# Performance work log

Measured on AMD Instinct MI355X. Metric: run time of the kernel, lower is better.

Reference implementation:

```python
import jax, jax.numpy as jnp
import numpy as np

NUM_HEADS = 64  # init kwarg


def _split_heads(x, num_heads):
    # torch: x.view(N, num_heads, head_size).permute(0, 2, 1) -> [N, head_size, num_heads]
    n, hidden = x.shape
    head_size = hidden // num_heads
    return x.reshape(n, num_heads, head_size).transpose(0, 2, 1)


def setup_inputs() -> dict:
    key = jax.random.key(0)
    kq, kk, kv = jax.random.split(key, 3)
    N, H = 4096, 4096
    q = jax.random.normal(kq, (N, H), dtype=jnp.float32)
    k = jax.random.normal(kk, (N, H), dtype=jnp.float32)
    v = jax.random.normal(kv, (N, H), dtype=jnp.float32)
    return {"q": q, "k": k, "v": v}


def reference(q, k, v):
    n, hidden = q.shape
    qh = _split_heads(q, NUM_HEADS)  # [N, d, h] with d=head_size, h=num_heads
    kh = _split_heads(k, NUM_HEADS)
    vh = _split_heads(v, NUM_HEADS)
    # scores: contraction over the num_heads axis (faithful to the original code)
    scores = jnp.einsum('ndh,neh->nde', qh, kh)      # [N, d, d]
    probs = jax.nn.softmax(scores, axis=-1)           # softmax over last dim, no scaling
    out = jnp.einsum('nde,neh->ndh', probs, vh)       # [N, d, h]
    # permute(0,2,1) then flatten -> [N, hidden]
    return out.transpose(0, 2, 1).reshape(n, hidden)
```

## Files before the change

### kernel.cpp

```cpp
#include <hip/hip_runtime.h>
#include <hip/hip_bf16.h>

typedef __bf16 bf16x8 __attribute__((ext_vector_type(8)));
typedef float  f32x4  __attribute__((ext_vector_type(4)));
typedef short  s16x8  __attribute__((ext_vector_type(8)));
typedef unsigned short u16;

static __device__ __forceinline__ u16 f2bf_rne(float f) {
  union { float f; unsigned u; } x; x.f = f;
  unsigned r = x.u + 0x7fffu + ((x.u >> 16) & 1u);
  return (u16)(r >> 16);
}

static __device__ __forceinline__ void splitbf(float f, short& hi, short& lo) {
  union { float f; unsigned u; } x; x.f = f;
  hi = (short)(x.u >> 16);
  union { unsigned u; float f; } h; h.u = x.u & 0xffff0000u;
  union { float f; unsigned u; } y; y.f = f - h.f;
  lo = (short)(y.u >> 16);
}

#define GLD_LDS16(g, l)                                                        \
  __builtin_amdgcn_global_load_lds(                                            \
      (const __attribute__((address_space(1))) void*)(g),                      \
      (__attribute__((address_space(3))) void*)(l), 16, 0, 0)

__global__ __launch_bounds__(256, 3)
void attn64_kernel(const float* __restrict__ q, const float* __restrict__ k,
                   const float* __restrict__ v, float* __restrict__ out)
{
  __shared__ float ldsQ[4096];
  __shared__ float ldsK[4096];
  __shared__ float ldsV[4096];

  const int tid  = threadIdx.x;
  const int wid  = tid >> 6;
  const int lane = tid & 63;
  const int quad = lane >> 4;
  const int lo   = lane & 15;
  const int row  = blockIdx.x;

  const float* qrow = q + (size_t)row * 4096;
  const float* krow = k + (size_t)row * 4096;
  const float* vrow = v + (size_t)row * 4096;
  float*       orow = out + (size_t)row * 4096;

  {
    const int hl = lane >> 4;
    const int e4 = (lane & 15) << 2;
#pragma unroll
    for (int i = 0; i < 4; ++i) {
      const int c = wid * 4 + i;
      const int h = c * 4 + hl;
      const int seQK = e4 ^ (((h >> 3) & 1) << 4);
      const int seV  = e4 ^ ((h & 15) << 2);
      GLD_LDS16(qrow + h * 64 + seQK, &ldsQ[c * 256]);
      GLD_LDS16(krow + h * 64 + seQK, &ldsK[c * 256]);
      GLD_LDS16(vrow + h * 64 + seV,  &ldsV[c * 256]);
    }
  }
  __syncthreads();

  s16x8 qh[2], ql[2];
  {
    const int dcol = wid * 16 + lo;
#pragma unroll
    for (int ks = 0; ks < 2; ++ks)
#pragma unroll
      for (int j = 0; j < 8; ++j) {
        const int h = ks * 32 + quad * 8 + j;
        float x = ldsQ[h * 64 + (dcol ^ ((quad & 1) << 4))];
        short hh, ll; splitbf(x, hh, ll);
        qh[ks][j] = hh; ql[ks][j] = ll;
      }
  }

  f32x4 acc[4];
#pragma unroll
  for (int et = 0; et < 4; ++et) acc[et] = (f32x4){0.f, 0.f, 0.f, 0.f};

#pragma unroll
  for (int et = 0; et < 4; ++et)
#pragma unroll
    for (int ks = 0; ks < 2; ++ks) {
      s16x8 kh, kl;
#pragma unroll
      for (int j = 0; j < 8; ++j) {
        const int h = ks * 32 + quad * 8 + j;
        float x = ldsK[h * 64 + ((lo + 16 * et) ^ ((quad & 1) << 4))];
        short hh, ll; splitbf(x, hh, ll);
        kh[j] = hh; kl[j] = ll;
      }
      bf16x8 ah = __builtin_bit_cast(bf16x8, qh[ks]);
      bf16x8 al = __builtin_bit_cast(bf16x8, ql[ks]);
      bf16x8 bh = __builtin_bit_cast(bf16x8, kh);
      bf16x8 bl = __builtin_bit_cast(bf16x8, kl);
      acc[et] = __builtin_amdgcn_mfma_f32_16x16x32_bf16(ah, bh, acc[et], 0, 0, 0);
      acc[et] = __builtin_amdgcn_mfma_f32_16x16x32_bf16(ah, bl, acc[et], 0, 0, 0);
      acc[et] = __builtin_amdgcn_mfma_f32_16x16x32_bf16(al, bh, acc[et], 0, 0, 0);
    }

#pragma unroll
  for (int r = 0; r < 4; ++r) {
    float m = fmaxf(fmaxf(acc[0][r], acc[1][r]), fmaxf(acc[2][r], acc[3][r]));
#pragma unroll
    for (int off = 1; off < 16; off <<= 1) m = fmaxf(m, __shfl_xor(m, off));
    float s = 0.f;
#pragma unroll
    for (int et = 0; et < 4; ++et) {
      float e0 = __expf(acc[et][r] - m);
      acc[et][r] = e0;
      s += e0;
    }
#pragma unroll
    for (int off = 1; off < 16; off <<= 1) s += __shfl_xor(s, off);
    float rs = 1.0f / s;
#pragma unroll
    for (int et = 0; et < 4; ++et) acc[et][r] *= rs;
  }

  __syncthreads();

  float* P = ldsK;
#pragma unroll
  for (int r = 0; r < 4; ++r) {
    const int d   = wid * 16 + quad * 4 + r;
    const int swz = (d & 15) << 2;
#pragma unroll
    for (int et = 0; et < 4; ++et)
      P[d * 64 + ((lo + 16 * et) ^ swz)] = acc[et][r];
  }

  f32x4 acc2[4];
#pragma unroll
  for (int mt = 0; mt < 4; ++mt) acc2[mt] = (f32x4){0.f, 0.f, 0.f, 0.f};

#pragma unroll
  for (int ks = 0; ks < 2; ++ks) {
    const int eb = quad * 8 + ks * 32;

    const int dmine = wid * 16 + lo;
    const int pswz  = lo << 2;
    f32x4 p0 = *(const f32x4*)&P[dmine * 64 + (eb ^ pswz)];
    f32x4 p1 = *(const f32x4*)&P[dmine * 64 + ((eb + 4) ^ pswz)];
    s16x8 tp;
#pragma unroll
    for (int j = 0; j < 4; ++j) {
      tp[j]     = (short)f2bf_rne(p0[j]);
      tp[4 + j] = (short)f2bf_rne(p1[j]);
    }
    bf16x8 bp = __builtin_bit_cast(bf16x8, tp);

#pragma unroll
    for (int mt = 0; mt < 4; ++mt) {
      const int h    = lo + 16 * mt;
      const int vswz = lo << 2;
      f32x4 v0 = *(const f32x4*)&ldsV[h * 64 + (eb ^ vswz)];
      f32x4 v1 = *(const f32x4*)&ldsV[h * 64 + ((eb + 4) ^ vswz)];
      s16x8 tv;
#pragma unroll
      for (int j = 0; j < 4; ++j) {
        tv[j]     = (short)f2bf_rne(v0[j]);
        tv[4 + j] = (short)f2bf_rne(v1[j]);
      }
      bf16x8 av = __builtin_bit_cast(bf16x8, tv);
      acc2[mt] = __builtin_amdgcn_mfma_f32_16x16x32_bf16(av, bp, acc2[mt], 0, 0, 0);
    }
  }

#pragma unroll
  for (int mt = 0; mt < 4; ++mt)
#pragma unroll
    for (int r = 0; r < 4; ++r) {
      const int h = 16 * mt + quad * 4 + r;
      orow[h * 64 + wid * 16 + lo] = acc2[mt][r];
    }
}

extern "C" void kernel_launch(void* const* d_in, const int* in_sizes, int n_in,
                              void* d_out, int out_size, void* d_ws, size_t ws_size,
                              hipStream_t stream) {
  const float* q = (const float*)d_in[0];
  const float* k = (const float*)d_in[1];
  const float* v = (const float*)d_in[2];
  float* o = (float*)d_out;
  hipLaunchKernelGGL(attn64_kernel, dim3(4096), dim3(256), 0, stream, q, k, v, o);
}
```

Measured before the change: 213.4 us.

## Process eight rows per block with double-buffered async Q/K staging and register V

Each 512-thread block now handles 8 rows, two at a time over 4 iterations. While one LDS buffer is being computed on, Q/K for the next pair of rows stream into the other buffer through global_load_lds, and V is loaded straight into registers instead of going through LDS. The aim is to hide global-load latency behind MFMA and softmax work and to cut per-block launch overhead. The cost is more LDS (128KB per block, so fewer resident blocks), high register pressure from holding V in registers, and hand-written barriers and waitcnt that are easy to get wrong.

```diff
diff --git a/kernel.cpp b/kernel.cpp
--- a/kernel.cpp
+++ b/kernel.cpp
@@ -25,156 +25,183 @@
       (const __attribute__((address_space(1))) void*)(g),                      \
       (__attribute__((address_space(3))) void*)(l), 16, 0, 0)
 
-__global__ __launch_bounds__(256, 3)
+__global__ __launch_bounds__(512, 2)
 void attn64_kernel(const float* __restrict__ q, const float* __restrict__ k,
                    const float* __restrict__ v, float* __restrict__ out)
 {
-  __shared__ float ldsQ[4096];
-  __shared__ float ldsK[4096];
-  __shared__ float ldsV[4096];
+  __shared__ float lds[2][2][2][4096];
 
   const int tid  = threadIdx.x;
   const int wid  = tid >> 6;
   const int lane = tid & 63;
   const int quad = lane >> 4;
   const int lo   = lane & 15;
-  const int row  = blockIdx.x;
-
-  const float* qrow = q + (size_t)row * 4096;
-  const float* krow = k + (size_t)row * 4096;
-  const float* vrow = v + (size_t)row * 4096;
-  float*       orow = out + (size_t)row * 4096;
-
-  {
+  const int rw   = wid >> 2;
+  const int wq   = wid & 3;
+  const int rowBase = blockIdx.x * 8;
+
+  auto stage = [&](int t, int b) {
     const int hl = lane >> 4;
     const int e4 = (lane & 15) << 2;
 #pragma unroll
-    for (int i = 0; i < 4; ++i) {
-      const int c = wid * 4 + i;
-      const int h = c * 4 + hl;
-      const int seQK = e4 ^ (((h >> 3) & 1) << 4);
-      const int seV  = e4 ^ ((h & 15) << 2);
-      GLD_LDS16(qrow + h * 64 + seQK, &ldsQ[c * 256]);
-      GLD_LDS16(krow + h * 64 + seQK, &ldsK[c * 256]);
-      GLD_LDS16(vrow + h * 64 + seV,  &ldsV[c * 256]);
-    }
+    for (int i = 0; i < 8; ++i) {
+      const int c   = wid * 8 + i;
+      const int sec = c >> 4;
+      const int c4  = c & 15;
+      const int h   = c4 * 4 + hl;
+      const int se  = e4 ^ (((h >> 3) & 1) << 4);
+      const float* src = ((sec & 1) ? k : q)
+                       + (size_t)(rowBase + t * 2 + (sec >> 1)) * 4096
+                       + h * 64 + se;
+      GLD_LDS16(src, &lds[b][sec & 1][sec >> 1][c4 * 256]);
+    }
+  };
+
+  f32x4 xv[8][2];
+  auto loadV = [&](int t) {
+    const float* vrow = v + (size_t)(rowBase + t * 2 + rw) * 4096;
+#pragma unroll
+    for (int ks = 0; ks < 2; ++ks)
+#pragma unroll
+      for (int mt = 0; mt < 4; ++mt) {
+        const float* p = vrow + (lo + 16 * mt) * 64 + quad * 8 + ks * 32;
+        xv[ks * 4 + mt][0] = *(const f32x4*)p;
+        xv[ks * 4 + mt][1] = *(const f32x4*)(p + 4);
+      }
+  };
+
+  stage(0, 0);
+  loadV(0);
+
+  for (int t = 0; t < 4; ++t) {
+    const int b = t & 1;
+
+    asm volatile("s_waitcnt vmcnt(0)\n\ts_barrier" ::: "memory");
+    __builtin_amdgcn_sched_barrier(0);
+
+    bf16x8 av[8];
+#pragma unroll
+    for (int i = 0; i < 8; ++i) {
+      s16x8 tv;
+#pragma unroll
+      for (int j = 0; j < 4; ++j) {
+        tv[j]     = (short)f2bf_rne(xv[i][0][j]);
+        tv[4 + j] = (short)f2bf_rne(xv[i][1][j]);
+      }
+      av[i] = __builtin_bit_cast(bf16x8, tv);
+    }
+
+    if (t < 3) {
+      stage(t + 1, b ^ 1);
+      loadV(t + 1);
+    }
+
+    const float* ldsQ = &lds[b][0][rw][0];
+    float*       ldsK = &lds[b][1][rw][0];
+
+    s16x8 qh[2], ql[2];
+    {
+      const int dcol = wq * 16 + lo;
+#pragma unroll
+      for (int ks = 0; ks < 2; ++ks)
+#pragma unroll
+        for (int j = 0; j < 8; ++j) {
+          const int h = ks * 32 + quad * 8 + j;
+          float x = ldsQ[h * 64 + (dcol ^ ((quad & 1) << 4))];
+          short hh, ll; splitbf(x, hh, ll);
+          qh[ks][j] = hh; ql[ks][j] = ll;
+        }
+    }
+
+    f32x4 acc[4];
+#pragma unroll
+    for (int et = 0; et < 4; ++et) acc[et] = (f32x4){0.f, 0.f, 0.f, 0.f};
+
+#pragma unroll
+    for (int et = 0; et < 4; ++et)
+#pragma unroll
+      for (int ks = 0; ks < 2; ++ks) {
+        s16x8 kh, kl;
+#pragma unroll
+        for (int j = 0; j < 8; ++j) {
+          const int h = ks * 32 + quad * 8 + j;
+          float x = ldsK[h * 64 + ((lo + 16 * et) ^ ((quad & 1) << 4))];
+          short hh, ll; splitbf(x, hh, ll);
+          kh[j] = hh; kl[j] = ll;
+        }
+        bf16x8 ah = __builtin_bit_cast(bf16x8, qh[ks]);
+        bf16x8 al = __builtin_bit_cast(bf16x8, ql[ks]);
+        bf16x8 bh = __builtin_bit_cast(bf16x8, kh);
+        bf16x8 bl = __builtin_bit_cast(bf16x8, kl);
+        acc[et] = __builtin_amdgcn_mfma_f32_16x16x32_bf16(ah, bh, acc[et], 0, 0, 0);
+        acc[et] = __builtin_amdgcn_mfma_f32_16x16x32_bf16(ah, bl, acc[et], 0, 0, 0);
+        acc[et] = __builtin_amdgcn_mfma_f32_16x16x32_bf16(al, bh, acc[et], 0, 0, 0);
+      }
+
+#pragma unroll
+    for (int r = 0; r < 4; ++r) {
+      float m = fmaxf(fmaxf(acc[0][r], acc[1][r]), fmaxf(acc[2][r], acc[3][r]));
+#pragma unroll
+      for (int off = 1; off < 16; off <<= 1) m = fmaxf(m, __shfl_xor(m, off));
+      float s = 0.f;
+#pragma unroll
+      for (int et = 0; et < 4; ++et) {
+        float e0 = __expf(acc[et][r] - m);
+        acc[et][r] = e0;
+        s += e0;
+      }
+#pragma unroll
+      for (int off = 1; off < 16; off <<= 1) s += __shfl_xor(s, off);
+      float rs = 1.0f / s;
+#pragma unroll
+      for (int et = 0; et < 4; ++et) acc[et][r] *= rs;
+    }
+
+    asm volatile("s_barrier" ::: "memory");
+    __builtin_amdgcn_sched_barrier(0);
+
+    float* P = ldsK;
+#pragma unroll
+    for (int r = 0; r < 4; ++r) {
+      const int d   = wq * 16 + quad * 4 + r;
+      const int swz = (d & 15) << 2;
+#pragma unroll
+      for (int et = 0; et < 4; ++et)
+        P[d * 64 + ((lo + 16 * et) ^ swz)] = acc[et][r];
+    }
+
+    f32x4 acc2[4];
+#pragma unroll
+    for (int mt = 0; mt < 4; ++mt) acc2[mt] = (f32x4){0.f, 0.f, 0.f, 0.f};
+
+#pragma unroll
+    for (int ks = 0; ks < 2; ++ks) {
+      const int eb    = quad * 8 + ks * 32;
+      const int dmine = wq * 16 + lo;
+      const int pswz  = lo << 2;
+      f32x4 p0 = *(const f32x4*)&P[dmine * 64 + (eb ^ pswz)];
+      f32x4 p1 = *(const f32x4*)&P[dmine * 64 + ((eb + 4) ^ pswz)];
+      s16x8 tp;
+#pragma unroll
+      for (int j = 0; j < 4; ++j) {
+        tp[j]     = (short)f2bf_rne(p0[j]);
+        tp[4 + j] = (short)f2bf_rne(p1[j]);
+      }
+      bf16x8 bp = __builtin_bit_cast(bf16x8, tp);
+#pragma unroll
+      for (int mt = 0; mt < 4; ++mt)
+        acc2[mt] = __builtin_amdgcn_mfma_f32_16x16x32_bf16(av[ks * 4 + mt], bp, acc2[mt], 0, 0, 0);
+    }
+
+    float* orow = out + (size_t)(rowBase + t * 2 + rw) * 4096;
+#pragma unroll
+    for (int mt = 0; mt < 4; ++mt)
+#pragma unroll
+      for (int r = 0; r < 4; ++r) {
+        const int h = 16 * mt + quad * 4 + r;
+        orow[h * 64 + wq * 16 + lo] = acc2[mt][r];
+      }
   }
-  __syncthreads();
-
-  s16x8 qh[2], ql[2];
-  {
-    const int dcol = wid * 16 + lo;
-#pragma unroll
-    for (int ks = 0; ks < 2; ++ks)
-#pragma unroll
-      for (int j = 0; j < 8; ++j) {
-        const int h = ks * 32 + quad * 8 + j;
-        float x = ldsQ[h * 64 + (dcol ^ ((quad & 1) << 4))];
-        short hh, ll; splitbf(x, hh, ll);
-        qh[ks][j] = hh; ql[ks][j] = ll;
-      }
-  }
-
-  f32x4 acc[4];
-#pragma unroll
-  for (int et = 0; et < 4; ++et) acc[et] = (f32x4){0.f, 0.f, 0.f, 0.f};
-
-#pragma unroll
-  for (int et = 0; et < 4; ++et)
-#pragma unroll
-    for (int ks = 0; ks < 2; ++ks) {
-      s16x8 kh, kl;
-#pragma unroll
-      for (int j = 0; j < 8; ++j) {
-        const int h = ks * 32 + quad * 8 + j;
-        float x = ldsK[h * 64 + ((lo + 16 * et) ^ ((quad & 1) << 4))];
-        short hh, ll; splitbf(x, hh, ll);
-        kh[j] = hh; kl[j] = ll;
-      }
-      bf16x8 ah = __builtin_bit_cast(bf16x8, qh[ks]);
-      bf16x8 al = __builtin_bit_cast(bf16x8, ql[ks]);
-      bf16x8 bh = __builtin_bit_cast(bf16x8, kh);
-      bf16x8 bl = __builtin_bit_cast(bf16x8, kl);
-      acc[et] = __builtin_amdgcn_mfma_f32_16x16x32_bf16(ah, bh, acc[et], 0, 0, 0);
-      acc[et] = __builtin_amdgcn_mfma_f32_16x16x32_bf16(ah, bl, acc[et], 0, 0, 0);
-      acc[et] = __builtin_amdgcn_mfma_f32_16x16x32_bf16(al, bh, acc[et], 0, 0, 0);
-    }
-
-#pragma unroll
-  for (int r = 0; r < 4; ++r) {
-    float m = fmaxf(fmaxf(acc[0][r], acc[1][r]), fmaxf(acc[2][r], acc[3][r]));
-#pragma unroll
-    for (int off = 1; off < 16; off <<= 1) m = fmaxf(m, __shfl_xor(m, off));
-    float s = 0.f;
-#pragma unroll
-    for (int et = 0; et < 4; ++et) {
-      float e0 = __expf(acc[et][r] - m);
-      acc[et][r] = e0;
-      s += e0;
-    }
-#pragma unroll
-    for (int off = 1; off < 16; off <<= 1) s += __shfl_xor(s, off);
-    float rs = 1.0f / s;
-#pragma unroll
-    for (int et = 0; et < 4; ++et) acc[et][r] *= rs;
-  }
-
-  __syncthreads();
-
-  float* P = ldsK;
-#pragma unroll
-  for (int r = 0; r < 4; ++r) {
-    const int d   = wid * 16 + quad * 4 + r;
-    const int swz = (d & 15) << 2;
-#pragma unroll
-    for (int et = 0; et < 4; ++et)
-      P[d * 64 + ((lo + 16 * et) ^ swz)] = acc[et][r];
-  }
-
-  f32x4 acc2[4];
-#pragma unroll
-  for (int mt = 0; mt < 4; ++mt) acc2[mt] = (f32x4){0.f, 0.f, 0.f, 0.f};
-
-#pragma unroll
-  for (int ks = 0; ks < 2; ++ks) {
-    const int eb = quad * 8 + ks * 32;
-
-    const int dmine = wid * 16 + lo;
-    const int pswz  = lo << 2;
-    f32x4 p0 = *(const f32x4*)&P[dmine * 64 + (eb ^ pswz)];
-    f32x4 p1 = *(const f32x4*)&P[dmine * 64 + ((eb + 4) ^ pswz)];
-    s16x8 tp;
-#pragma unroll
-    for (int j = 0; j < 4; ++j) {
-      tp[j]     = (short)f2bf_rne(p0[j]);
-      tp[4 + j] = (short)f2bf_rne(p1[j]);
-    }
-    bf16x8 bp = __builtin_bit_cast(bf16x8, tp);
-
-#pragma unroll
-    for (int mt = 0; mt < 4; ++mt) {
-      const int h    = lo + 16 * mt;
-      const int vswz = lo << 2;
-      f32x4 v0 = *(const f32x4*)&ldsV[h * 64 + (eb ^ vswz)];
-      f32x4 v1 = *(const f32x4*)&ldsV[h * 64 + ((eb + 4) ^ vswz)];
-      s16x8 tv;
-#pragma unroll
-      for (int j = 0; j < 4; ++j) {
-        tv[j]     = (short)f2bf_rne(v0[j]);
-        tv[4 + j] = (short)f2bf_rne(v1[j]);
-      }
-      bf16x8 av = __builtin_bit_cast(bf16x8, tv);
-      acc2[mt] = __builtin_amdgcn_mfma_f32_16x16x32_bf16(av, bp, acc2[mt], 0, 0, 0);
-    }
-  }
-
-#pragma unroll
-  for (int mt = 0; mt < 4; ++mt)
-#pragma unroll
-    for (int r = 0; r < 4; ++r) {
-      const int h = 16 * mt + quad * 4 + r;
-      orow[h * 64 + wid * 16 + lo] = acc2[mt][r];
-    }
 }
 
 extern "C" void kernel_launch(void* const* d_in, const int* in_sizes, int n_in,
@@ -184,5 +211,5 @@
   const float* k = (const float*)d_in[1];
   const float* v = (const float*)d_in[2];
   float* o = (float*)d_out;
-  hipLaunchKernelGGL(attn64_kernel, dim3(4096), dim3(256), 0, stream, q, k, v, o);
-}
+  hipLaunchKernelGGL(attn64_kernel, dim3(512), dim3(512), 0, stream, q, k, v, o);
+}
```

Result: slower. 233.3 us (+9.3%).

## Load V directly into registers, drop V LDS buffer, raise occupancy

Applied to the files above, without the earlier changes.

V is no longer staged through shared memory. Each thread issues direct global vector loads of its V fragments into registers right after the Q/K LDS fill, and converts them to bf16 just before the second MFMA stage. This cuts LDS use per block from 48KB to 32KB, and launch bounds are raised to 4 blocks per CU so more rows can be in flight. The cost is 64 extra VGPRs held live across the QK^T and softmax phases, which may cause spills or limit occupancy under the tighter register budget. The direct V loads are also less coalesced than the previous LDS-staged path.

```diff
diff --git a/kernel.cpp b/kernel.cpp
--- a/kernel.cpp
+++ b/kernel.cpp
@@ -25,13 +25,12 @@
       (const __attribute__((address_space(1))) void*)(g),                      \
       (__attribute__((address_space(3))) void*)(l), 16, 0, 0)
 
-__global__ __launch_bounds__(256, 3)
+__global__ __launch_bounds__(256, 4)
 void attn64_kernel(const float* __restrict__ q, const float* __restrict__ k,
                    const float* __restrict__ v, float* __restrict__ out)
 {
   __shared__ float ldsQ[4096];
   __shared__ float ldsK[4096];
-  __shared__ float ldsV[4096];
 
   const int tid  = threadIdx.x;
   const int wid  = tid >> 6;
@@ -49,17 +48,28 @@
     const int hl = lane >> 4;
     const int e4 = (lane & 15) << 2;
 #pragma unroll
-    for (int i = 0; i < 4; ++i) {
-      const int c = wid * 4 + i;
-      const int h = c * 4 + hl;
-      const int seQK = e4 ^ (((h >> 3) & 1) << 4);
-      const int seV  = e4 ^ ((h & 15) << 2);
-      GLD_LDS16(qrow + h * 64 + seQK, &ldsQ[c * 256]);
-      GLD_LDS16(krow + h * 64 + seQK, &ldsK[c * 256]);
-      GLD_LDS16(vrow + h * 64 + seV,  &ldsV[c * 256]);
+    for (int i = 0; i < 8; ++i) {
+      const int c   = wid * 8 + i;
+      const int sec = c >> 4;
+      const int c4  = c & 15;
+      const int h   = c4 * 4 + hl;
+      const int se  = e4 ^ (((h >> 3) & 1) << 4);
+      const float* src = (sec ? krow : qrow) + h * 64 + se;
+      GLD_LDS16(src, (sec ? ldsK : ldsQ) + c4 * 256);
     }
   }
   __syncthreads();
+
+  f32x4 xv[8][2];
+#pragma unroll
+  for (int ks = 0; ks < 2; ++ks)
+#pragma unroll
+    for (int mt = 0; mt < 4; ++mt) {
+      const float* p = vrow + (lo + 16 * mt) * 64 + quad * 8 + ks * 32;
+      xv[ks * 4 + mt][0] = *(const f32x4*)p;
+      xv[ks * 4 + mt][1] = *(const f32x4*)(p + 4);
+    }
+  __builtin_amdgcn_sched_barrier(0);
 
   s16x8 qh[2], ql[2];
   {
@@ -121,6 +131,18 @@
 
   __syncthreads();
 
+  bf16x8 av[8];
+#pragma unroll
+  for (int i = 0; i < 8; ++i) {
+    s16x8 tv;
+#pragma unroll
+    for (int j = 0; j < 4; ++j) {
+      tv[j]     = (short)f2bf_rne(xv[i][0][j]);
+      tv[4 + j] = (short)f2bf_rne(xv[i][1][j]);
+    }
+    av[i] = __builtin_bit_cast(bf16x8, tv);
+  }
+
   float* P = ldsK;
 #pragma unroll
   for (int r = 0; r < 4; ++r) {
@@ -137,8 +159,7 @@
 
 #pragma unroll
   for (int ks = 0; ks < 2; ++ks) {
-    const int eb = quad * 8 + ks * 32;
-
+    const int eb    = quad * 8 + ks * 32;
     const int dmine = wid * 16 + lo;
     const int pswz  = lo << 2;
     f32x4 p0 = *(const f32x4*)&P[dmine * 64 + (eb ^ pswz)];
@@ -150,22 +171,9 @@
       tp[4 + j] = (short)f2bf_rne(p1[j]);
     }
     bf16x8 bp = __builtin_bit_cast(bf16x8, tp);
-
 #pragma unroll
-    for (int mt = 0; mt < 4; ++mt) {
-      const int h    = lo + 16 * mt;
-      const int vswz = lo << 2;
-      f32x4 v0 = *(const f32x4*)&ldsV[h * 64 + (eb ^ vswz)];
-      f32x4 v1 = *(const f32x4*)&ldsV[h * 64 + ((eb + 4) ^ vswz)];
-      s16x8 tv;
-#pragma unroll
-      for (int j = 0; j < 4; ++j) {
-        tv[j]     = (short)f2bf_rne(v0[j]);
-        tv[4 + j] = (short)f2bf_rne(v1[j]);
-      }
-      bf16x8 av = __builtin_bit_cast(bf16x8, tv);
-      acc2[mt] = __builtin_amdgcn_mfma_f32_16x16x32_bf16(av, bp, acc2[mt], 0, 0, 0);
-    }
+    for (int mt = 0; mt < 4; ++mt)
+      acc2[mt] = __builtin_amdgcn_mfma_f32_16x16x32_bf16(av[ks * 4 + mt], bp, acc2[mt], 0, 0, 0);
   }
 
 #pragma unroll
```

Result: no change. 215.6 us (+1.0%).
